# Kernel tuning notes

Measured on AMD Instinct MI355X. Metric: run time of the kernel, lower is better.

Reference implementation:

```python
import jax, jax.numpy as jnp
import numpy as np
from jax import lax

K = 3          # kernel_size
STRIDE = 1
PAD = 1
DIL = 1


def conv2d(x, w, b):
    y = lax.conv_general_dilated(
        x, w, (STRIDE, STRIDE), [(PAD, PAD), (PAD, PAD)],
        rhs_dilation=(DIL, DIL),
        dimension_numbers=('NCHW', 'OIHW', 'NCHW'))
    return y + b[None, :, None, None]


def setup_inputs() -> dict:
    key = jax.random.key(0)
    ks = jax.random.split(key, 6)
    N, Cin, Cout, H, W = 4, 64, 64, 192, 192
    K2 = K * K
    x_input = jax.random.normal(ks[0], (N, Cin, H, W), jnp.float32)
    # offset branch: 2*K2 output channels (dy, dx per kernel tap); small init
    w_off = jax.random.normal(ks[1], (2 * K2, Cin, K, K), jnp.float32) * 0.01
    b_off = jnp.zeros((2 * K2,), jnp.float32)
    # modulation branch (DCNv2): K2 channels, 2*sigmoid
    w_mod = jax.random.normal(ks[2], (K2, Cin, K, K), jnp.float32) * 0.01
    b_mod = jnp.zeros((K2,), jnp.float32)
    # main conv weight + bias
    w = jax.random.normal(ks[3], (Cout, Cin, K, K), jnp.float32) / np.sqrt(Cin * K2)
    b = jax.random.normal(ks[4], (Cout,), jnp.float32) * 0.01
    return {'x_input': x_input, 'w_off': w_off, 'b_off': b_off,
            'w_mod': w_mod, 'b_mod': b_mod, 'w': w, 'b': b}


def _deform_sample(x, py, px):
    # x [N,C,H,W]; py,px [N,K2,Ho,Wo] -> bilinear samples [N,C,K2,Ho,Wo]
    N, C, H, W = x.shape
    xf = x.reshape(N, C, H * W)
    y0 = jnp.floor(py)
    x0 = jnp.floor(px)
    ly = py - y0
    lx = px - x0
    y0i = y0.astype(jnp.int32)
    x0i = x0.astype(jnp.int32)

    def gather(yi, xi, wt):
        valid = (yi >= 0) & (yi < H) & (xi >= 0) & (xi < W)  # zero padding outside
        idx = jnp.clip(yi, 0, H - 1) * W + jnp.clip(xi, 0, W - 1)
        idx_flat = idx.reshape(N, -1)
        vals = jax.vmap(lambda a, i: jnp.take(a, i, axis=1))(xf, idx_flat)  # [N,C,K2*Ho*Wo]
        vals = vals.reshape(N, C, *yi.shape[1:])
        return vals * (wt * valid)[:, None]

    out = gather(y0i, x0i, (1 - ly) * (1 - lx))
    out = out + gather(y0i, x0i + 1, (1 - ly) * lx)
    out = out + gather(y0i + 1, x0i, ly * (1 - lx))
    out = out + gather(y0i + 1, x0i + 1, ly * lx)
    return out


def reference(x_input, w_off, b_off, w_mod, b_mod, w, b):
    N, C, H, W = x_input.shape
    K2 = K * K
    off = conv2d(x_input, w_off, b_off)                       # [N,2*K2,Ho,Wo]
    mod = 2.0 * jax.nn.sigmoid(conv2d(x_input, w_mod, b_mod))  # [N,K2,Ho,Wo]
    Ho, Wo = off.shape[2], off.shape[3]
    off = off.reshape(N, K2, 2, Ho, Wo)
    ky = jnp.repeat(jnp.arange(K) * DIL, K).astype(jnp.float32)  # [K2]
    kx = jnp.tile(jnp.arange(K) * DIL, K).astype(jnp.float32)
    hy = (jnp.arange(Ho) * STRIDE - PAD).astype(jnp.float32)
    wx = (jnp.arange(Wo) * STRIDE - PAD).astype(jnp.float32)
    py = off[:, :, 0] + hy[None, None, :, None] + ky[None, :, None, None]  # [N,K2,Ho,Wo]
    px = off[:, :, 1] + wx[None, None, None, :] + kx[None, :, None, None]
    val = _deform_sample(x_input, py, px) * mod[:, None]       # [N,C,K2,Ho,Wo]
    out = jnp.einsum('nckhw,ock->nohw', val, w.reshape(w.shape[0], C, K2))
    out = out + b[None, :, None, None]
    return jax.nn.relu(out)
```

## Files before the change

kernel.cpp:

```cpp
#include <hip/hip_runtime.h>
#include <hip/hip_bf16.h>
#include <hip/hip_fp16.h>
#include <math.h>


#define NB   4
#define CIN  64
#define COUT 64
#define HH   192
#define WW   192
#define HW   (HH*WW)

typedef __attribute__((ext_vector_type(4))) float f32x4;
typedef __attribute__((ext_vector_type(8))) _Float16 f16x8;
typedef __attribute__((ext_vector_type(4))) unsigned int u32x4;

__device__ __forceinline__ int iclamp(int v, int lo, int hi) {
    return v < lo ? lo : (v > hi ? hi : v);
}
__device__ __forceinline__ unsigned short f16bits(float f) {
    __half h = __float2half(f);
    union { __half h; unsigned short u; } t; t.h = h; return t.u;
}
__device__ __forceinline__ float h2f(unsigned short u) {
    union { unsigned short u; __half h; } t; t.u = u; return __half2float(t.h);
}

__global__ __launch_bounds__(256) void to_nhwc(
        const float* __restrict__ x, unsigned short* __restrict__ xt) {
    int n  = blockIdx.y;
    int px = blockIdx.x * 256 + threadIdx.x;
    const float* xn = x + (size_t)n * CIN * HW + px;
    union { unsigned short us[64]; u32x4 q[8]; } pk;
#pragma unroll
    for (int c = 0; c < 64; c++) pk.us[c] = f16bits(xn[c * HW]);
    u32x4* dst = (u32x4*)(xt + ((size_t)n * HW + px) * 64);
#pragma unroll
    for (int i = 0; i < 8; i++) dst[i] = pk.q[i];
}

__global__ __launch_bounds__(256) void prep_weights(
        const float* __restrict__ w, const float* __restrict__ w_off,
        const float* __restrict__ w_mod, const float* __restrict__ b_off,
        const float* __restrict__ b_mod, unsigned short* __restrict__ wfrag,
        unsigned short* __restrict__ wauxf, float* __restrict__ baux) {
    int idx = blockIdx.x * 256 + threadIdx.x;
    if (idx < 36864) {
        int j    = idx & 7;
        int lane = (idx >> 3) & 63;
        int kc   = (idx >> 9) & 1;
        int g    = (idx >> 10) & 3;
        int k    = idx >> 12;
        int o = g * 16 + (lane & 15);
        int c = kc * 32 + (lane >> 4) * 8 + j;
        wfrag[idx] = f16bits(w[(o * 64 + c) * 9 + k]);
    }
    if (idx < 18432) {
        int j    = idx & 7;
        int lane = (idx >> 3) & 63;
        int kc   = (idx >> 9) & 1;
        int ga   = (idx >> 10) & 1;
        int k    = idx >> 11;
        int o = ga * 16 + (lane & 15);
        int c = kc * 32 + (lane >> 4) * 8 + j;
        float v = 0.f;
        if (o < 18)      v = w_off[(o * 64 + c) * 9 + k];
        else if (o < 27) v = w_mod[((o - 18) * 64 + c) * 9 + k];
        wauxf[idx] = f16bits(v);
    }
    if (idx < 32) {
        float v = 0.f;
        if (idx < 18)      v = b_off[idx];
        else if (idx < 27) v = b_mod[idx - 18];
        baux[idx] = v;
    }
}

__global__ __launch_bounds__(256, 4) void dcn_fused(
        const unsigned short* __restrict__ xt,
        const unsigned short* __restrict__ wfrag,
        const unsigned short* __restrict__ wauxf,
        const float* __restrict__ baux,
        const float* __restrict__ bias,
        float* __restrict__ out) {
    __shared__ __align__(16) unsigned short win[216 * 64];
    __shared__ unsigned short oml[2][32][34];

    int tid = threadIdx.x;
    int l   = tid & 63;
    int wv  = __builtin_amdgcn_readfirstlane(tid >> 6);
    int r2  = wv >> 1;
    int g2  = wv & 1;

    int id = blockIdx.x;
    int sw = (id & 7) * 288 + (id >> 3);
    int n  = sw / 576;
    int r  = sw % 576;
    int ho2    = (r / 6) * 2;
    int wobase = (r % 6) * 32;

    const char* xb = (const char*)xt + (size_t)n * HW * 128;

    if (tid < 216) {
        int rw = tid / 36, cl = tid - rw * 36;
        int gy = iclamp(ho2 - 2 + rw, 0, HH - 1);
        int gx = iclamp(wobase - 2 + cl, 0, WW - 1);
        const u32x4* src = (const u32x4*)(xb + ((size_t)gy * WW + gx) * 128);
        char* dst = (char*)win + tid * 128;
        int xw = (tid & 7) << 4;
#pragma unroll
        for (int c = 0; c < 8; c++)
            *(u32x4*)(dst + ((c * 16) ^ xw)) = src[c];
    }
    __syncthreads();

    {
        f32x4 aacc[2];
        aacc[0] = (f32x4){0.f, 0.f, 0.f, 0.f};
        aacc[1] = (f32x4){0.f, 0.f, 0.f, 0.f};
        const f16x8 zero8 = (f16x8){0, 0, 0, 0, 0, 0, 0, 0};
        int pa   = g2 * 16 + (l & 15);
        int cba  = (l >> 4) * 16;
        int ho_w = ho2 + r2;

#pragma unroll 1
        for (int k = 0; k < 9; k++) {
            int ky = k / 3, kx = k - 3 * (k / 3);
            int ys = ho_w + ky - 1;
            if ((unsigned)ys >= (unsigned)HH) continue;
            int xs = wobase + pa + kx - 1;
            bool ok = (unsigned)xs < (unsigned)WW;
            int sA = (ky + 1 + r2) * 36 + (pa + kx + 1);
            const char* pp = (const char*)win + sA * 128;
            int xw = (sA & 7) << 4;
            const f16x8* wa = ((const f16x8*)wauxf) + (k * 4) * 64 + l;
#pragma unroll
            for (int kc = 0; kc < 2; kc++) {
                f16x8 bv = *(const f16x8*)(pp + ((kc * 64 + cba) ^ xw));
                if (!ok) bv = zero8;
                f16x8 a0 = wa[(kc)     * 64];
                f16x8 a1 = wa[(2 + kc) * 64];
                aacc[0] = __builtin_amdgcn_mfma_f32_16x16x32_f16(a0, bv, aacc[0], 0, 0, 0);
                aacc[1] = __builtin_amdgcn_mfma_f32_16x16x32_f16(a1, bv, aacc[1], 0, 0, 0);
            }
        }
#pragma unroll
        for (int h = 0; h < 2; h++) {
#pragma unroll
            for (int rr = 0; rr < 4; rr++) {
                int o = h * 16 + (l >> 4) * 4 + rr;
                float v = aacc[h][rr] + baux[o];
                if (o >= 18) v = 2.f / (1.f + expf(-v));
                oml[r2][o][pa] = f16bits(v);
            }
        }
    }
    __syncthreads();

    f32x4 acc[4];
#pragma unroll
    for (int nf = 0; nf < 4; nf++) acc[nf] = (f32x4){0.f, 0.f, 0.f, 0.f};

    int p_loc = l & 15;
    int chunk = l >> 4;
    int p     = g2 * 16 + p_loc;
    int ho_w  = ho2 + r2;
    int wox   = wobase + p;
    int cb0   = chunk * 16;

    union Q { u32x4 u; __half2 h2[4]; };

#pragma unroll 1
    for (int k = 0; k < 9; k++) {
        const f16x8* wfk = ((const f16x8*)wfrag) + (k * 8) * 64 + l;
        f16x8 wB[8];
#pragma unroll
        for (int f = 0; f < 8; f++) wB[f] = wfk[f * 64];

        int ky = k / 3, kx = k - 3 * (k / 3);
        float offy = h2f(oml[r2][2 * k][p]);
        float offx = h2f(oml[r2][2 * k + 1][p]);
        float mm   = h2f(oml[r2][18 + k][p]);
        float py  = offy + (float)(ho_w - 1 + ky);
        float pxf = offx + (float)(wox - 1 + kx);
        float y0f = floorf(py), x0f = floorf(pxf);
        float ly = py - y0f, lx = pxf - x0f;
        int y0 = (int)y0f, x0 = (int)x0f;
        int y1 = y0 + 1, x1 = x0 + 1;
        bool y0ok = (unsigned)y0 < (unsigned)HH, y1ok = (unsigned)y1 < (unsigned)HH;
        bool x0ok = (unsigned)x0 < (unsigned)WW, x1ok = (unsigned)x1 < (unsigned)WW;
        float wt0 = (y0ok && x0ok) ? mm * (1.f - ly) * (1.f - lx) : 0.f;
        float wt1 = (y0ok && x1ok) ? mm * (1.f - ly) * lx         : 0.f;
        float wt2 = (y1ok && x0ok) ? mm * ly * (1.f - lx)         : 0.f;
        float wt3 = (y1ok && x1ok) ? mm * ly * lx                 : 0.f;
        int y0c = iclamp(y0, 0, HH - 1), y1c = iclamp(y1, 0, HH - 1);
        int x0c = iclamp(x0, 0, WW - 1), x1c = iclamp(x1, 0, WW - 1);

        int sy0 = y0c - ho2 + 2,    sy1 = y1c - ho2 + 2;
        int sx0 = x0c - wobase + 2, sx1 = x1c - wobase + 2;
        int sy0c = iclamp(sy0, 0, 5),  sy1c = iclamp(sy1, 0, 5);
        int sx0c = iclamp(sx0, 0, 35), sx1c = iclamp(sx1, 0, 35);
        bool fb00 = (wt0 > 0.f) && ((sy0 != sy0c) | (sx0 != sx0c));
        bool fb01 = (wt1 > 0.f) && ((sy0 != sy0c) | (sx1 != sx1c));
        bool fb10 = (wt2 > 0.f) && ((sy1 != sy1c) | (sx0 != sx0c));
        bool fb11 = (wt3 > 0.f) && ((sy1 != sy1c) | (sx1 != sx1c));

        int s00 = sy0c * 36 + sx0c, s01 = sy0c * 36 + sx1c;
        int s10 = sy1c * 36 + sx0c, s11 = sy1c * 36 + sx1c;
        const char* w00 = (const char*)win + s00 * 128;
        const char* w01 = (const char*)win + s01 * 128;
        const char* w10 = (const char*)win + s10 * 128;
        const char* w11 = (const char*)win + s11 * 128;
        int x00 = (s00 & 7) << 4, x01 = (s01 & 7) << 4;
        int x10 = (s10 & 7) << 4, x11 = (s11 & 7) << 4;
        Q q0, q1, q2, q3, q4, q5, q6, q7;
        q0.u = *(const u32x4*)(w00 + ((cb0)      ^ x00));
        q1.u = *(const u32x4*)(w00 + ((cb0 + 64) ^ x00));
        q2.u = *(const u32x4*)(w01 + ((cb0)      ^ x01));
        q3.u = *(const u32x4*)(w01 + ((cb0 + 64) ^ x01));
        q4.u = *(const u32x4*)(w10 + ((cb0)      ^ x10));
        q5.u = *(const u32x4*)(w10 + ((cb0 + 64) ^ x10));
        q6.u = *(const u32x4*)(w11 + ((cb0)      ^ x11));
        q7.u = *(const u32x4*)(w11 + ((cb0 + 64) ^ x11));

        if (__builtin_expect(fb00 | fb01 | fb10 | fb11, 0)) {
            if (fb00) { const char* gp = xb + ((size_t)y0c * WW + x0c) * 128 + cb0;
                        q0.u = *(const u32x4*)gp; q1.u = *(const u32x4*)(gp + 64); }
            if (fb01) { const char* gp = xb + ((size_t)y0c * WW + x1c) * 128 + cb0;
                        q2.u = *(const u32x4*)gp; q3.u = *(const u32x4*)(gp + 64); }
            if (fb10) { const char* gp = xb + ((size_t)y1c * WW + x0c) * 128 + cb0;
                        q4.u = *(const u32x4*)gp; q5.u = *(const u32x4*)(gp + 64); }
            if (fb11) { const char* gp = xb + ((size_t)y1c * WW + x1c) * 128 + cb0;
                        q6.u = *(const u32x4*)gp; q7.u = *(const u32x4*)(gp + 64); }
        }

        __half2 wv0 = __float2half2_rn(wt0);
        __half2 wv1 = __float2half2_rn(wt1);
        __half2 wv2 = __float2half2_rn(wt2);
        __half2 wv3 = __float2half2_rn(wt3);
        union { __half2 h2[4]; f16x8 v; } fA0, fA1;
#pragma unroll
        for (int j = 0; j < 4; j++) {
            __half2 t = __hmul2(q0.h2[j], wv0);
            t = __hfma2(q2.h2[j], wv1, t);
            t = __hfma2(q4.h2[j], wv2, t);
            t = __hfma2(q6.h2[j], wv3, t);
            fA0.h2[j] = t;
            __half2 s = __hmul2(q1.h2[j], wv0);
            s = __hfma2(q3.h2[j], wv1, s);
            s = __hfma2(q5.h2[j], wv2, s);
            s = __hfma2(q7.h2[j], wv3, s);
            fA1.h2[j] = s;
        }

        __builtin_amdgcn_s_setprio(1);
#pragma unroll
        for (int nf = 0; nf < 4; nf++) {
            acc[nf] = __builtin_amdgcn_mfma_f32_16x16x32_f16(fA0.v, wB[nf * 2],     acc[nf], 0, 0, 0);
            acc[nf] = __builtin_amdgcn_mfma_f32_16x16x32_f16(fA1.v, wB[nf * 2 + 1], acc[nf], 0, 0, 0);
        }
        __builtin_amdgcn_s_setprio(0);
    }

#pragma unroll
    for (int nf = 0; nf < 4; nf++) {
        int o = nf * 16 + p_loc;
        float bo = bias[o];
        int wo = wobase + g2 * 16 + chunk * 4;
        float* op = out + (((size_t)n * COUT + o) * HH + ho_w) * WW + wo;
#pragma unroll
        for (int rr = 0; rr < 4; rr++) {
            float v = acc[nf][rr] + bo;
            op[rr] = fmaxf(v, 0.f);
        }
    }
}

extern "C" void kernel_launch(void* const* d_in, const int* in_sizes, int n_in,
                              void* d_out, int out_size, void* d_ws, size_t ws_size,
                              hipStream_t stream) {
    const float* x     = (const float*)d_in[0];
    const float* w_off = (const float*)d_in[1];
    const float* b_off = (const float*)d_in[2];
    const float* w_mod = (const float*)d_in[3];
    const float* b_mod = (const float*)d_in[4];
    const float* w     = (const float*)d_in[5];
    const float* b     = (const float*)d_in[6];
    float* out = (float*)d_out;

    unsigned short* wfrag = (unsigned short*)d_ws;
    unsigned short* wauxf = wfrag + 36864;
    float* baux = (float*)(wauxf + 18432);
    unsigned short* xt = (unsigned short*)(baux + 32);

    to_nhwc<<<dim3(144, NB), dim3(256), 0, stream>>>(x, xt);
    prep_weights<<<dim3(144), dim3(256), 0, stream>>>(w, w_off, w_mod, b_off,
                                                      b_mod, wfrag, wauxf, baux);
    dcn_fused<<<dim3(2304), dim3(256), 0, stream>>>(xt, wfrag, wauxf, baux, b, out);
}
```

Measured before the change: 71.27 us.

## Retile DCN block to 4 rows by 16 columns with coalesced halo load

Each block now covers a 4x16 output tile instead of 2x32, which shrinks the shared-memory halo window from 216 to 160 pixels and cuts redundant halo loads. The window fill is rewritten so all 256 threads load 16-byte chunks across five passes instead of 216 threads each copying a full pixel. Launch bounds rise to 6 blocks per CU for more occupancy, which tightens the register budget and may cause spills.

```diff
diff --git a/kernel.cpp b/kernel.cpp
--- a/kernel.cpp
+++ b/kernel.cpp
@@ -76,41 +76,40 @@
     }
 }
 
-__global__ __launch_bounds__(256, 4) void dcn_fused(
+__global__ __launch_bounds__(256, 6) void dcn_fused(
         const unsigned short* __restrict__ xt,
         const unsigned short* __restrict__ wfrag,
         const unsigned short* __restrict__ wauxf,
         const float* __restrict__ baux,
         const float* __restrict__ bias,
         float* __restrict__ out) {
-    __shared__ __align__(16) unsigned short win[216 * 64];
-    __shared__ unsigned short oml[2][32][34];
+    __shared__ __align__(16) unsigned short win[160 * 64];
+    __shared__ unsigned short oml[4][32][17];
 
     int tid = threadIdx.x;
     int l   = tid & 63;
-    int wv  = __builtin_amdgcn_readfirstlane(tid >> 6);
-    int r2  = wv >> 1;
-    int g2  = wv & 1;
+    int r4  = __builtin_amdgcn_readfirstlane(tid >> 6);
 
     int id = blockIdx.x;
     int sw = (id & 7) * 288 + (id >> 3);
     int n  = sw / 576;
     int r  = sw % 576;
-    int ho2    = (r / 6) * 2;
-    int wobase = (r % 6) * 32;
+    int ho4    = (r / 12) * 4;
+    int wobase = (r % 12) * 16;
 
     const char* xb = (const char*)xt + (size_t)n * HW * 128;
 
-    if (tid < 216) {
-        int rw = tid / 36, cl = tid - rw * 36;
-        int gy = iclamp(ho2 - 2 + rw, 0, HH - 1);
-        int gx = iclamp(wobase - 2 + cl, 0, WW - 1);
-        const u32x4* src = (const u32x4*)(xb + ((size_t)gy * WW + gx) * 128);
-        char* dst = (char*)win + tid * 128;
-        int xw = (tid & 7) << 4;
-#pragma unroll
-        for (int c = 0; c < 8; c++)
-            *(u32x4*)(dst + ((c * 16) ^ xw)) = src[c];
+    {
+        int part = tid & 7;
+#pragma unroll
+        for (int pass = 0; pass < 5; pass++) {
+            int slot = (pass * 256 + tid) >> 3;
+            int rw = slot / 20, cl = slot - rw * 20;
+            int gy = iclamp(ho4 - 2 + rw, 0, HH - 1);
+            int gx = iclamp(wobase - 2 + cl, 0, WW - 1);
+            u32x4 v = *(const u32x4*)(xb + ((size_t)gy * WW + gx) * 128 + part * 16);
+            *(u32x4*)((char*)win + slot * 128 + ((part * 16) ^ ((slot & 7) << 4))) = v;
+        }
     }
     __syncthreads();
 
@@ -119,9 +118,9 @@
         aacc[0] = (f32x4){0.f, 0.f, 0.f, 0.f};
         aacc[1] = (f32x4){0.f, 0.f, 0.f, 0.f};
         const f16x8 zero8 = (f16x8){0, 0, 0, 0, 0, 0, 0, 0};
-        int pa   = g2 * 16 + (l & 15);
+        int pa   = l & 15;
         int cba  = (l >> 4) * 16;
-        int ho_w = ho2 + r2;
+        int ho_w = ho4 + r4;
 
 #pragma unroll 1
         for (int k = 0; k < 9; k++) {
@@ -130,7 +129,7 @@
             if ((unsigned)ys >= (unsigned)HH) continue;
             int xs = wobase + pa + kx - 1;
             bool ok = (unsigned)xs < (unsigned)WW;
-            int sA = (ky + 1 + r2) * 36 + (pa + kx + 1);
+            int sA = (r4 + ky + 1) * 20 + (pa + kx + 1);
             const char* pp = (const char*)win + sA * 128;
             int xw = (sA & 7) << 4;
             const f16x8* wa = ((const f16x8*)wauxf) + (k * 4) * 64 + l;
@@ -151,7 +150,7 @@
                 int o = h * 16 + (l >> 4) * 4 + rr;
                 float v = aacc[h][rr] + baux[o];
                 if (o >= 18) v = 2.f / (1.f + expf(-v));
-                oml[r2][o][pa] = f16bits(v);
+                oml[r4][o][pa] = f16bits(v);
             }
         }
     }
@@ -163,9 +162,8 @@
 
     int p_loc = l & 15;
     int chunk = l >> 4;
-    int p     = g2 * 16 + p_loc;
-    int ho_w  = ho2 + r2;
-    int wox   = wobase + p;
+    int ho_w  = ho4 + r4;
+    int wox   = wobase + p_loc;
     int cb0   = chunk * 16;
 
     union Q { u32x4 u; __half2 h2[4]; };
@@ -178,9 +176,9 @@
         for (int f = 0; f < 8; f++) wB[f] = wfk[f * 64];
 
         int ky = k / 3, kx = k - 3 * (k / 3);
-        float offy = h2f(oml[r2][2 * k][p]);
-        float offx = h2f(oml[r2][2 * k + 1][p]);
-        float mm   = h2f(oml[r2][18 + k][p]);
+        float offy = h2f(oml[r4][2 * k][p_loc]);
+        float offx = h2f(oml[r4][2 * k + 1][p_loc]);
+        float mm   = h2f(oml[r4][18 + k][p_loc]);
         float py  = offy + (float)(ho_w - 1 + ky);
         float pxf = offx + (float)(wox - 1 + kx);
         float y0f = floorf(py), x0f = floorf(pxf);
@@ -196,17 +194,17 @@
         int y0c = iclamp(y0, 0, HH - 1), y1c = iclamp(y1, 0, HH - 1);
         int x0c = iclamp(x0, 0, WW - 1), x1c = iclamp(x1, 0, WW - 1);
 
-        int sy0 = y0c - ho2 + 2,    sy1 = y1c - ho2 + 2;
+        int sy0 = y0c - ho4 + 2,    sy1 = y1c - ho4 + 2;
         int sx0 = x0c - wobase + 2, sx1 = x1c - wobase + 2;
-        int sy0c = iclamp(sy0, 0, 5),  sy1c = iclamp(sy1, 0, 5);
-        int sx0c = iclamp(sx0, 0, 35), sx1c = iclamp(sx1, 0, 35);
+        int sy0c = iclamp(sy0, 0, 7),  sy1c = iclamp(sy1, 0, 7);
+        int sx0c = iclamp(sx0, 0, 19), sx1c = iclamp(sx1, 0, 19);
         bool fb00 = (wt0 > 0.f) && ((sy0 != sy0c) | (sx0 != sx0c));
         bool fb01 = (wt1 > 0.f) && ((sy0 != sy0c) | (sx1 != sx1c));
         bool fb10 = (wt2 > 0.f) && ((sy1 != sy1c) | (sx0 != sx0c));
         bool fb11 = (wt3 > 0.f) && ((sy1 != sy1c) | (sx1 != sx1c));
 
-        int s00 = sy0c * 36 + sx0c, s01 = sy0c * 36 + sx1c;
-        int s10 = sy1c * 36 + sx0c, s11 = sy1c * 36 + sx1c;
+        int s00 = sy0c * 20 + sx0c, s01 = sy0c * 20 + sx1c;
+        int s10 = sy1c * 20 + sx0c, s11 = sy1c * 20 + sx1c;
         const char* w00 = (const char*)win + s00 * 128;
         const char* w01 = (const char*)win + s01 * 128;
         const char* w10 = (const char*)win + s10 * 128;
@@ -266,7 +264,7 @@
     for (int nf = 0; nf < 4; nf++) {
         int o = nf * 16 + p_loc;
         float bo = bias[o];
-        int wo = wobase + g2 * 16 + chunk * 4;
+        int wo = wobase + chunk * 4;
         float* op = out + (((size_t)n * COUT + o) * HH + ho_w) * WW + wo;
 #pragma unroll
         for (int rr = 0; rr < 4; rr++) {
```

After: 134.6 us. +88.9%, slower.

## Software-pipeline bilinear gather one tap ahead of MFMA in deform conv

Applied to the files above, without the earlier changes.

Splits the per-tap loop into a STAGE phase (offset decode, weight computation, LDS gathers) and a CONSUME phase (blend and MFMA). Stages are double-buffered so the gather for tap k+1 is issued before the MFMAs for tap k, with sched_barriers keeping that order. The offset/mask LDS layout is transposed so each pixel's dy,dx pair can be read as one 32-bit load. The extra live registers are covered by lowering launch bounds from 4 to 3 blocks per SIMD, which risks lower occupancy.

```diff
diff --git a/kernel.cpp b/kernel.cpp
--- a/kernel.cpp
+++ b/kernel.cpp
@@ -76,7 +76,99 @@
     }
 }
 
-__global__ __launch_bounds__(256, 4) void dcn_fused(
+union Qreg { u32x4 u; __half2 h2[4]; };
+
+#define STAGE(K, WT, Q) do {                                                  \
+    int k_ = (K);                                                             \
+    int ky_ = k_ / 3, kx_ = k_ - 3 * (k_ / 3);                                \
+    unsigned int oyx_ = *(const unsigned int*)(omp + 2 * k_);                 \
+    float offy_ = h2f((unsigned short)(oyx_ & 0xffffu));                      \
+    float offx_ = h2f((unsigned short)(oyx_ >> 16));                          \
+    float mm_   = h2f(omp[18 + k_]);                                          \
+    float py_  = offy_ + (float)(ho_w - 1 + ky_);                             \
+    float pxf_ = offx_ + (float)(wox - 1 + kx_);                              \
+    float y0f_ = floorf(py_), x0f_ = floorf(pxf_);                            \
+    float ly_ = py_ - y0f_, lx_ = pxf_ - x0f_;                                \
+    int y0_ = (int)y0f_, x0_ = (int)x0f_;                                     \
+    int y1_ = y0_ + 1, x1_ = x0_ + 1;                                         \
+    bool y0ok_ = (unsigned)y0_ < (unsigned)HH, y1ok_ = (unsigned)y1_ < (unsigned)HH; \
+    bool x0ok_ = (unsigned)x0_ < (unsigned)WW, x1ok_ = (unsigned)x1_ < (unsigned)WW; \
+    float wt0_ = (y0ok_ && x0ok_) ? mm_ * (1.f - ly_) * (1.f - lx_) : 0.f;    \
+    float wt1_ = (y0ok_ && x1ok_) ? mm_ * (1.f - ly_) * lx_         : 0.f;    \
+    float wt2_ = (y1ok_ && x0ok_) ? mm_ * ly_ * (1.f - lx_)         : 0.f;    \
+    float wt3_ = (y1ok_ && x1ok_) ? mm_ * ly_ * lx_                 : 0.f;    \
+    WT[0] = __float2half2_rn(wt0_);                                           \
+    WT[1] = __float2half2_rn(wt1_);                                           \
+    WT[2] = __float2half2_rn(wt2_);                                           \
+    WT[3] = __float2half2_rn(wt3_);                                           \
+    int y0c_ = iclamp(y0_, 0, HH - 1), y1c_ = iclamp(y1_, 0, HH - 1);         \
+    int x0c_ = iclamp(x0_, 0, WW - 1), x1c_ = iclamp(x1_, 0, WW - 1);         \
+    int sy0_ = y0c_ - ho2 + 2,    sy1_ = y1c_ - ho2 + 2;                      \
+    int sx0_ = x0c_ - wobase + 2, sx1_ = x1c_ - wobase + 2;                   \
+    int sy0c_ = iclamp(sy0_, 0, 5),  sy1c_ = iclamp(sy1_, 0, 5);              \
+    int sx0c_ = iclamp(sx0_, 0, 35), sx1c_ = iclamp(sx1_, 0, 35);             \
+    bool fb00_ = (wt0_ > 0.f) && ((sy0_ != sy0c_) | (sx0_ != sx0c_));         \
+    bool fb01_ = (wt1_ > 0.f) && ((sy0_ != sy0c_) | (sx1_ != sx1c_));         \
+    bool fb10_ = (wt2_ > 0.f) && ((sy1_ != sy1c_) | (sx0_ != sx0c_));         \
+    bool fb11_ = (wt3_ > 0.f) && ((sy1_ != sy1c_) | (sx1_ != sx1c_));         \
+    int s00_ = sy0c_ * 36 + sx0c_, s01_ = sy0c_ * 36 + sx1c_;                 \
+    int s10_ = sy1c_ * 36 + sx0c_, s11_ = sy1c_ * 36 + sx1c_;                 \
+    const char* w00_ = (const char*)win + s00_ * 128;                         \
+    const char* w01_ = (const char*)win + s01_ * 128;                         \
+    const char* w10_ = (const char*)win + s10_ * 128;                         \
+    const char* w11_ = (const char*)win + s11_ * 128;                         \
+    int x00_ = (s00_ & 7) << 4, x01_ = (s01_ & 7) << 4;                       \
+    int x10_ = (s10_ & 7) << 4, x11_ = (s11_ & 7) << 4;                       \
+    Q[0].u = *(const u32x4*)(w00_ + ((cb0)      ^ x00_));                     \
+    Q[1].u = *(const u32x4*)(w00_ + ((cb0 + 64) ^ x00_));                     \
+    Q[2].u = *(const u32x4*)(w01_ + ((cb0)      ^ x01_));                     \
+    Q[3].u = *(const u32x4*)(w01_ + ((cb0 + 64) ^ x01_));                     \
+    Q[4].u = *(const u32x4*)(w10_ + ((cb0)      ^ x10_));                     \
+    Q[5].u = *(const u32x4*)(w10_ + ((cb0 + 64) ^ x10_));                     \
+    Q[6].u = *(const u32x4*)(w11_ + ((cb0)      ^ x11_));                     \
+    Q[7].u = *(const u32x4*)(w11_ + ((cb0 + 64) ^ x11_));                     \
+    if (__builtin_expect(fb00_ | fb01_ | fb10_ | fb11_, 0)) {                 \
+        if (fb00_) { const char* gp = xb + ((size_t)y0c_ * WW + x0c_) * 128 + cb0; \
+                     Q[0].u = *(const u32x4*)gp; Q[1].u = *(const u32x4*)(gp + 64); } \
+        if (fb01_) { const char* gp = xb + ((size_t)y0c_ * WW + x1c_) * 128 + cb0; \
+                     Q[2].u = *(const u32x4*)gp; Q[3].u = *(const u32x4*)(gp + 64); } \
+        if (fb10_) { const char* gp = xb + ((size_t)y1c_ * WW + x0c_) * 128 + cb0; \
+                     Q[4].u = *(const u32x4*)gp; Q[5].u = *(const u32x4*)(gp + 64); } \
+        if (fb11_) { const char* gp = xb + ((size_t)y1c_ * WW + x1c_) * 128 + cb0; \
+                     Q[6].u = *(const u32x4*)gp; Q[7].u = *(const u32x4*)(gp + 64); } \
+    }                                                                         \
+} while (0)
+
+#define CONSUME(K, WT, Q) do {                                                \
+    int k_ = (K);                                                             \
+    const f16x8* wfk_ = ((const f16x8*)wfrag) + (k_ * 8) * 64 + l;            \
+    f16x8 wB_[8];                                                             \
+    _Pragma("unroll")                                                         \
+    for (int f_ = 0; f_ < 8; ++f_) wB_[f_] = wfk_[f_ * 64];                   \
+    union { __half2 h2[4]; f16x8 v; } fA0_, fA1_;                             \
+    _Pragma("unroll")                                                         \
+    for (int j_ = 0; j_ < 4; ++j_) {                                          \
+        __half2 t_ = __hmul2(Q[0].h2[j_], WT[0]);                             \
+        t_ = __hfma2(Q[2].h2[j_], WT[1], t_);                                 \
+        t_ = __hfma2(Q[4].h2[j_], WT[2], t_);                                 \
+        t_ = __hfma2(Q[6].h2[j_], WT[3], t_);                                 \
+        fA0_.h2[j_] = t_;                                                     \
+        __half2 s_ = __hmul2(Q[1].h2[j_], WT[0]);                             \
+        s_ = __hfma2(Q[3].h2[j_], WT[1], s_);                                 \
+        s_ = __hfma2(Q[5].h2[j_], WT[2], s_);                                 \
+        s_ = __hfma2(Q[7].h2[j_], WT[3], s_);                                 \
+        fA1_.h2[j_] = s_;                                                     \
+    }                                                                         \
+    __builtin_amdgcn_s_setprio(1);                                            \
+    _Pragma("unroll")                                                         \
+    for (int nf_ = 0; nf_ < 4; ++nf_) {                                       \
+        acc[nf_] = __builtin_amdgcn_mfma_f32_16x16x32_f16(fA0_.v, wB_[nf_ * 2],     acc[nf_], 0, 0, 0); \
+        acc[nf_] = __builtin_amdgcn_mfma_f32_16x16x32_f16(fA1_.v, wB_[nf_ * 2 + 1], acc[nf_], 0, 0, 0); \
+    }                                                                         \
+    __builtin_amdgcn_s_setprio(0);                                            \
+} while (0)
+
+__global__ __launch_bounds__(256, 3) void dcn_fused(
         const unsigned short* __restrict__ xt,
         const unsigned short* __restrict__ wfrag,
         const unsigned short* __restrict__ wauxf,
@@ -84,7 +176,7 @@
         const float* __restrict__ bias,
         float* __restrict__ out) {
     __shared__ __align__(16) unsigned short win[216 * 64];
-    __shared__ unsigned short oml[2][32][34];
+    __shared__ __align__(16) unsigned short oml[2][32][32];
 
     int tid = threadIdx.x;
     int l   = tid & 63;
@@ -121,12 +213,12 @@
         const f16x8 zero8 = (f16x8){0, 0, 0, 0, 0, 0, 0, 0};
         int pa   = g2 * 16 + (l & 15);
         int cba  = (l >> 4) * 16;
-        int ho_w = ho2 + r2;
+        int ho_a = ho2 + r2;
 
 #pragma unroll 1
         for (int k = 0; k < 9; k++) {
             int ky = k / 3, kx = k - 3 * (k / 3);
-            int ys = ho_w + ky - 1;
+            int ys = ho_a + ky - 1;
             if ((unsigned)ys >= (unsigned)HH) continue;
             int xs = wobase + pa + kx - 1;
             bool ok = (unsigned)xs < (unsigned)WW;
@@ -151,7 +243,7 @@
                 int o = h * 16 + (l >> 4) * 4 + rr;
                 float v = aacc[h][rr] + baux[o];
                 if (o >= 18) v = 2.f / (1.f + expf(-v));
-                oml[r2][o][pa] = f16bits(v);
+                oml[r2][pa][o] = f16bits(v);
             }
         }
     }
@@ -167,100 +259,24 @@
     int ho_w  = ho2 + r2;
     int wox   = wobase + p;
     int cb0   = chunk * 16;
-
-    union Q { u32x4 u; __half2 h2[4]; };
-
+    const unsigned short* omp = &oml[r2][p][0];
+
+    __half2 wtA[4], wtB[4];
+    Qreg qA[8], qB[8];
+
+    STAGE(0, wtA, qA);
 #pragma unroll 1
-    for (int k = 0; k < 9; k++) {
-        const f16x8* wfk = ((const f16x8*)wfrag) + (k * 8) * 64 + l;
-        f16x8 wB[8];
-#pragma unroll
-        for (int f = 0; f < 8; f++) wB[f] = wfk[f * 64];
-
-        int ky = k / 3, kx = k - 3 * (k / 3);
-        float offy = h2f(oml[r2][2 * k][p]);
-        float offx = h2f(oml[r2][2 * k + 1][p]);
-        float mm   = h2f(oml[r2][18 + k][p]);
-        float py  = offy + (float)(ho_w - 1 + ky);
-        float pxf = offx + (float)(wox - 1 + kx);
-        float y0f = floorf(py), x0f = floorf(pxf);
-        float ly = py - y0f, lx = pxf - x0f;
-        int y0 = (int)y0f, x0 = (int)x0f;
-        int y1 = y0 + 1, x1 = x0 + 1;
-        bool y0ok = (unsigned)y0 < (unsigned)HH, y1ok = (unsigned)y1 < (unsigned)HH;
-        bool x0ok = (unsigned)x0 < (unsigned)WW, x1ok = (unsigned)x1 < (unsigned)WW;
-        float wt0 = (y0ok && x0ok) ? mm * (1.f - ly) * (1.f - lx) : 0.f;
-        float wt1 = (y0ok && x1ok) ? mm * (1.f - ly) * lx         : 0.f;
-        float wt2 = (y1ok && x0ok) ? mm * ly * (1.f - lx)         : 0.f;
-        float wt3 = (y1ok && x1ok) ? mm * ly * lx                 : 0.f;
-        int y0c = iclamp(y0, 0, HH - 1), y1c = iclamp(y1, 0, HH - 1);
-        int x0c = iclamp(x0, 0, WW - 1), x1c = iclamp(x1, 0, WW - 1);
-
-        int sy0 = y0c - ho2 + 2,    sy1 = y1c - ho2 + 2;
-        int sx0 = x0c - wobase + 2, sx1 = x1c - wobase + 2;
-        int sy0c = iclamp(sy0, 0, 5),  sy1c = iclamp(sy1, 0, 5);
-        int sx0c = iclamp(sx0, 0, 35), sx1c = iclamp(sx1, 0, 35);
-        bool fb00 = (wt0 > 0.f) && ((sy0 != sy0c) | (sx0 != sx0c));
-        bool fb01 = (wt1 > 0.f) && ((sy0 != sy0c) | (sx1 != sx1c));
-        bool fb10 = (wt2 > 0.f) && ((sy1 != sy1c) | (sx0 != sx0c));
-        bool fb11 = (wt3 > 0.f) && ((sy1 != sy1c) | (sx1 != sx1c));
-
-        int s00 = sy0c * 36 + sx0c, s01 = sy0c * 36 + sx1c;
-        int s10 = sy1c * 36 + sx0c, s11 = sy1c * 36 + sx1c;
-        const char* w00 = (const char*)win + s00 * 128;
-        const char* w01 = (const char*)win + s01 * 128;
-        const char* w10 = (const char*)win + s10 * 128;
-        const char* w11 = (const char*)win + s11 * 128;
-        int x00 = (s00 & 7) << 4, x01 = (s01 & 7) << 4;
-        int x10 = (s10 & 7) << 4, x11 = (s11 & 7) << 4;
-        Q q0, q1, q2, q3, q4, q5, q6, q7;
-        q0.u = *(const u32x4*)(w00 + ((cb0)      ^ x00));
-        q1.u = *(const u32x4*)(w00 + ((cb0 + 64) ^ x00));
-        q2.u = *(const u32x4*)(w01 + ((cb0)      ^ x01));
-        q3.u = *(const u32x4*)(w01 + ((cb0 + 64) ^ x01));
-        q4.u = *(const u32x4*)(w10 + ((cb0)      ^ x10));
-        q5.u = *(const u32x4*)(w10 + ((cb0 + 64) ^ x10));
-        q6.u = *(const u32x4*)(w11 + ((cb0)      ^ x11));
-        q7.u = *(const u32x4*)(w11 + ((cb0 + 64) ^ x11));
-
-        if (__builtin_expect(fb00 | fb01 | fb10 | fb11, 0)) {
-            if (fb00) { const char* gp = xb + ((size_t)y0c * WW + x0c) * 128 + cb0;
-                        q0.u = *(const u32x4*)gp; q1.u = *(const u32x4*)(gp + 64); }
-            if (fb01) { const char* gp = xb + ((size_t)y0c * WW + x1c) * 128 + cb0;
-                        q2.u = *(const u32x4*)gp; q3.u = *(const u32x4*)(gp + 64); }
-            if (fb10) { const char* gp = xb + ((size_t)y1c * WW + x0c) * 128 + cb0;
-                        q4.u = *(const u32x4*)gp; q5.u = *(const u32x4*)(gp + 64); }
-            if (fb11) { const char* gp = xb + ((size_t)y1c * WW + x1c) * 128 + cb0;
-                        q6.u = *(const u32x4*)gp; q7.u = *(const u32x4*)(gp + 64); }
-        }
-
-        __half2 wv0 = __float2half2_rn(wt0);
-        __half2 wv1 = __float2half2_rn(wt1);
-        __half2 wv2 = __float2half2_rn(wt2);
-        __half2 wv3 = __float2half2_rn(wt3);
-        union { __half2 h2[4]; f16x8 v; } fA0, fA1;
-#pragma unroll
-        for (int j = 0; j < 4; j++) {
-            __half2 t = __hmul2(q0.h2[j], wv0);
-            t = __hfma2(q2.h2[j], wv1, t);
-            t = __hfma2(q4.h2[j], wv2, t);
-            t = __hfma2(q6.h2[j], wv3, t);
-            fA0.h2[j] = t;
-            __half2 s = __hmul2(q1.h2[j], wv0);
-            s = __hfma2(q3.h2[j], wv1, s);
-            s = __hfma2(q5.h2[j], wv2, s);
-            s = __hfma2(q7.h2[j], wv3, s);
-            fA1.h2[j] = s;
-        }
-
-        __builtin_amdgcn_s_setprio(1);
-#pragma unroll
-        for (int nf = 0; nf < 4; nf++) {
-            acc[nf] = __builtin_amdgcn_mfma_f32_16x16x32_f16(fA0.v, wB[nf * 2],     acc[nf], 0, 0, 0);
-            acc[nf] = __builtin_amdgcn_mfma_f32_16x16x32_f16(fA1.v, wB[nf * 2 + 1], acc[nf], 0, 0, 0);
-        }
-        __builtin_amdgcn_s_setprio(0);
-    }
+    for (int kk = 0; kk < 4; ++kk) {
+        int k1 = 2 * kk + 1;
+        int k2 = 2 * kk + 2;
+        STAGE(k1, wtB, qB);
+        __builtin_amdgcn_sched_barrier(0);
+        CONSUME(2 * kk, wtA, qA);
+        STAGE(k2, wtA, qA);
+        __builtin_amdgcn_sched_barrier(0);
+        CONSUME(k1, wtB, qB);
+    }
+    CONSUME(8, wtA, qA);
 
 #pragma unroll
     for (int nf = 0; nf < 4; nf++) {
```

Result: slower. 75.60 us (+6.1%).

## Precompute deformable sampling plan once per pixel-tap in shared memory

Applied to the files above, without the earlier changes.

Before the change, each of the 4 lanes sharing a pixel (one per channel chunk) recomputed the bilinear coordinates, weights and fallback flags for every tap. Now a separate pass computes them once per (pixel, tap) across all 256 threads and stores them in shared memory: packed f16 weights plus signed indices, where a negative index marks a global-memory fallback. The main loop then only loads this plan and gathers. The oml layout is transposed so offsets can be read as packed pairs, and launch bounds drop from 4 to 3 waves per SIMD. The cost is an extra barrier, about 18KB more shared memory and lower occupancy.

```diff
diff --git a/kernel.cpp b/kernel.cpp
--- a/kernel.cpp
+++ b/kernel.cpp
@@ -14,6 +14,7 @@
 typedef __attribute__((ext_vector_type(4))) float f32x4;
 typedef __attribute__((ext_vector_type(8))) _Float16 f16x8;
 typedef __attribute__((ext_vector_type(4))) unsigned int u32x4;
+typedef __attribute__((ext_vector_type(4))) int i32x4;
 
 __device__ __forceinline__ int iclamp(int v, int lo, int hi) {
     return v < lo ? lo : (v > hi ? hi : v);
@@ -24,6 +25,10 @@
 }
 __device__ __forceinline__ float h2f(unsigned short u) {
     union { unsigned short u; __half h; } t; t.u = u; return __half2float(t.h);
+}
+__device__ __forceinline__ unsigned int dup16(float f) {
+    unsigned int b = f16bits(f);
+    return b | (b << 16);
 }
 
 __global__ __launch_bounds__(256) void to_nhwc(
@@ -76,7 +81,7 @@
     }
 }
 
-__global__ __launch_bounds__(256, 4) void dcn_fused(
+__global__ __launch_bounds__(256, 3) void dcn_fused(
         const unsigned short* __restrict__ xt,
         const unsigned short* __restrict__ wfrag,
         const unsigned short* __restrict__ wauxf,
@@ -84,7 +89,9 @@
         const float* __restrict__ bias,
         float* __restrict__ out) {
     __shared__ __align__(16) unsigned short win[216 * 64];
-    __shared__ unsigned short oml[2][32][34];
+    __shared__ __align__(16) unsigned short oml[2][32][32];
+    __shared__ __align__(16) u32x4 planW[576];
+    __shared__ __align__(16) i32x4 planC[576];
 
     int tid = threadIdx.x;
     int l   = tid & 63;
@@ -121,12 +128,12 @@
         const f16x8 zero8 = (f16x8){0, 0, 0, 0, 0, 0, 0, 0};
         int pa   = g2 * 16 + (l & 15);
         int cba  = (l >> 4) * 16;
-        int ho_w = ho2 + r2;
+        int ho_a = ho2 + r2;
 
 #pragma unroll 1
         for (int k = 0; k < 9; k++) {
             int ky = k / 3, kx = k - 3 * (k / 3);
-            int ys = ho_w + ky - 1;
+            int ys = ho_a + ky - 1;
             if ((unsigned)ys >= (unsigned)HH) continue;
             int xs = wobase + pa + kx - 1;
             bool ok = (unsigned)xs < (unsigned)WW;
@@ -147,42 +154,34 @@
 #pragma unroll
         for (int h = 0; h < 2; h++) {
 #pragma unroll
-            for (int rr = 0; rr < 4; rr++) {
-                int o = h * 16 + (l >> 4) * 4 + rr;
-                float v = aacc[h][rr] + baux[o];
-                if (o >= 18) v = 2.f / (1.f + expf(-v));
-                oml[r2][o][pa] = f16bits(v);
+            for (int rr = 0; rr < 2; rr++) {
+                int o = h * 16 + (l >> 4) * 4 + rr * 2;
+                float v0 = aacc[h][rr * 2]     + baux[o];
+                float v1 = aacc[h][rr * 2 + 1] + baux[o + 1];
+                if (o     >= 18) v0 = 2.f / (1.f + expf(-v0));
+                if (o + 1 >= 18) v1 = 2.f / (1.f + expf(-v1));
+                unsigned int pk = (unsigned int)f16bits(v0)
+                                | ((unsigned int)f16bits(v1) << 16);
+                *(unsigned int*)&oml[r2][pa][o] = pk;
             }
         }
     }
     __syncthreads();
 
-    f32x4 acc[4];
-#pragma unroll
-    for (int nf = 0; nf < 4; nf++) acc[nf] = (f32x4){0.f, 0.f, 0.f, 0.f};
-
-    int p_loc = l & 15;
-    int chunk = l >> 4;
-    int p     = g2 * 16 + p_loc;
-    int ho_w  = ho2 + r2;
-    int wox   = wobase + p;
-    int cb0   = chunk * 16;
-
-    union Q { u32x4 u; __half2 h2[4]; };
-
-#pragma unroll 1
-    for (int k = 0; k < 9; k++) {
-        const f16x8* wfk = ((const f16x8*)wfrag) + (k * 8) * 64 + l;
-        f16x8 wB[8];
-#pragma unroll
-        for (int f = 0; f < 8; f++) wB[f] = wfk[f * 64];
+    for (int i = tid; i < 576; i += 256) {
+        int rp = i / 9;
+        int k  = i - rp * 9;
+        int r2p = rp >> 5, px = rp & 31;
+        int ho_p  = ho2 + r2p;
+        int wox_p = wobase + px;
 
         int ky = k / 3, kx = k - 3 * (k / 3);
-        float offy = h2f(oml[r2][2 * k][p]);
-        float offx = h2f(oml[r2][2 * k + 1][p]);
-        float mm   = h2f(oml[r2][18 + k][p]);
-        float py  = offy + (float)(ho_w - 1 + ky);
-        float pxf = offx + (float)(wox - 1 + kx);
+        unsigned int oyx = *(const unsigned int*)&oml[r2p][px][2 * k];
+        float offy = h2f((unsigned short)(oyx & 0xffffu));
+        float offx = h2f((unsigned short)(oyx >> 16));
+        float mm   = h2f(oml[r2p][px][18 + k]);
+        float py  = offy + (float)(ho_p - 1 + ky);
+        float pxf = offx + (float)(wox_p - 1 + kx);
         float y0f = floorf(py), x0f = floorf(pxf);
         float ly = py - y0f, lx = pxf - x0f;
         int y0 = (int)y0f, x0 = (int)x0f;
@@ -195,61 +194,92 @@
         float wt3 = (y1ok && x1ok) ? mm * ly * lx                 : 0.f;
         int y0c = iclamp(y0, 0, HH - 1), y1c = iclamp(y1, 0, HH - 1);
         int x0c = iclamp(x0, 0, WW - 1), x1c = iclamp(x1, 0, WW - 1);
-
         int sy0 = y0c - ho2 + 2,    sy1 = y1c - ho2 + 2;
         int sx0 = x0c - wobase + 2, sx1 = x1c - wobase + 2;
         int sy0c = iclamp(sy0, 0, 5),  sy1c = iclamp(sy1, 0, 5);
         int sx0c = iclamp(sx0, 0, 35), sx1c = iclamp(sx1, 0, 35);
-        bool fb00 = (wt0 > 0.f) && ((sy0 != sy0c) | (sx0 != sx0c));
-        bool fb01 = (wt1 > 0.f) && ((sy0 != sy0c) | (sx1 != sx1c));
-        bool fb10 = (wt2 > 0.f) && ((sy1 != sy1c) | (sx0 != sx0c));
-        bool fb11 = (wt3 > 0.f) && ((sy1 != sy1c) | (sx1 != sx1c));
-
-        int s00 = sy0c * 36 + sx0c, s01 = sy0c * 36 + sx1c;
-        int s10 = sy1c * 36 + sx0c, s11 = sy1c * 36 + sx1c;
-        const char* w00 = (const char*)win + s00 * 128;
-        const char* w01 = (const char*)win + s01 * 128;
-        const char* w10 = (const char*)win + s10 * 128;
-        const char* w11 = (const char*)win + s11 * 128;
-        int x00 = (s00 & 7) << 4, x01 = (s01 & 7) << 4;
-        int x10 = (s10 & 7) << 4, x11 = (s11 & 7) << 4;
+        bool fb0 = (wt0 > 0.f) && ((sy0 != sy0c) | (sx0 != sx0c));
+        bool fb1 = (wt1 > 0.f) && ((sy0 != sy0c) | (sx1 != sx1c));
+        bool fb2 = (wt2 > 0.f) && ((sy1 != sy1c) | (sx0 != sx0c));
+        bool fb3 = (wt3 > 0.f) && ((sy1 != sy1c) | (sx1 != sx1c));
+        int c0 = fb0 ? -(y0c * WW + x0c) - 1 : sy0c * 36 + sx0c;
+        int c1 = fb1 ? -(y0c * WW + x1c) - 1 : sy0c * 36 + sx1c;
+        int c2 = fb2 ? -(y1c * WW + x0c) - 1 : sy1c * 36 + sx0c;
+        int c3 = fb3 ? -(y1c * WW + x1c) - 1 : sy1c * 36 + sx1c;
+
+        planW[i] = (u32x4){dup16(wt0), dup16(wt1), dup16(wt2), dup16(wt3)};
+        planC[i] = (i32x4){c0, c1, c2, c3};
+    }
+    __syncthreads();
+
+    f32x4 acc[4];
+#pragma unroll
+    for (int nf = 0; nf < 4; nf++) acc[nf] = (f32x4){0.f, 0.f, 0.f, 0.f};
+
+    int p_loc = l & 15;
+    int chunk = l >> 4;
+    int p     = g2 * 16 + p_loc;
+    int ho_w  = ho2 + r2;
+    int cb0   = chunk * 16;
+    int cb1   = cb0 + 64;
+    const char* planWp = (const char*)planW + (r2 * 32 + p) * 9 * 16;
+    const char* planCp = (const char*)planC + (r2 * 32 + p) * 9 * 16;
+
+    union Q { u32x4 u; __half2 h2[4]; };
+
+#pragma unroll 1
+    for (int k = 0; k < 9; k++) {
+        const f16x8* wfk = ((const f16x8*)wfrag) + (k * 8) * 64 + l;
+        f16x8 wB[8];
+#pragma unroll
+        for (int f = 0; f < 8; f++) wB[f] = wfk[f * 64];
+
+        union { u32x4 u; __half2 h2[4]; } pw;
+        pw.u = *(const u32x4*)(planWp + k * 16);
+        i32x4 pc = *(const i32x4*)(planCp + k * 16);
+        int c0 = pc.x, c1 = pc.y, c2 = pc.z, c3 = pc.w;
+
+        int d0 = c0 < 0 ? 0 : c0, d1 = c1 < 0 ? 0 : c1;
+        int d2 = c2 < 0 ? 0 : c2, d3 = c3 < 0 ? 0 : c3;
+        const char* b0 = (const char*)win + d0 * 128;
+        const char* b1 = (const char*)win + d1 * 128;
+        const char* b2 = (const char*)win + d2 * 128;
+        const char* b3 = (const char*)win + d3 * 128;
+        int x0 = (d0 & 7) << 4, x1 = (d1 & 7) << 4;
+        int x2 = (d2 & 7) << 4, x3 = (d3 & 7) << 4;
         Q q0, q1, q2, q3, q4, q5, q6, q7;
-        q0.u = *(const u32x4*)(w00 + ((cb0)      ^ x00));
-        q1.u = *(const u32x4*)(w00 + ((cb0 + 64) ^ x00));
-        q2.u = *(const u32x4*)(w01 + ((cb0)      ^ x01));
-        q3.u = *(const u32x4*)(w01 + ((cb0 + 64) ^ x01));
-        q4.u = *(const u32x4*)(w10 + ((cb0)      ^ x10));
-        q5.u = *(const u32x4*)(w10 + ((cb0 + 64) ^ x10));
-        q6.u = *(const u32x4*)(w11 + ((cb0)      ^ x11));
-        q7.u = *(const u32x4*)(w11 + ((cb0 + 64) ^ x11));
-
-        if (__builtin_expect(fb00 | fb01 | fb10 | fb11, 0)) {
-            if (fb00) { const char* gp = xb + ((size_t)y0c * WW + x0c) * 128 + cb0;
-                        q0.u = *(const u32x4*)gp; q1.u = *(const u32x4*)(gp + 64); }
-            if (fb01) { const char* gp = xb + ((size_t)y0c * WW + x1c) * 128 + cb0;
-                        q2.u = *(const u32x4*)gp; q3.u = *(const u32x4*)(gp + 64); }
-            if (fb10) { const char* gp = xb + ((size_t)y1c * WW + x0c) * 128 + cb0;
-                        q4.u = *(const u32x4*)gp; q5.u = *(const u32x4*)(gp + 64); }
-            if (fb11) { const char* gp = xb + ((size_t)y1c * WW + x1c) * 128 + cb0;
-                        q6.u = *(const u32x4*)gp; q7.u = *(const u32x4*)(gp + 64); }
-        }
-
-        __half2 wv0 = __float2half2_rn(wt0);
-        __half2 wv1 = __float2half2_rn(wt1);
-        __half2 wv2 = __float2half2_rn(wt2);
-        __half2 wv3 = __float2half2_rn(wt3);
+        q0.u = *(const u32x4*)(b0 + (cb0 ^ x0));
+        q1.u = *(const u32x4*)(b0 + (cb1 ^ x0));
+        q2.u = *(const u32x4*)(b1 + (cb0 ^ x1));
+        q3.u = *(const u32x4*)(b1 + (cb1 ^ x1));
+        q4.u = *(const u32x4*)(b2 + (cb0 ^ x2));
+        q5.u = *(const u32x4*)(b2 + (cb1 ^ x2));
+        q6.u = *(const u32x4*)(b3 + (cb0 ^ x3));
+        q7.u = *(const u32x4*)(b3 + (cb1 ^ x3));
+
+        if (__builtin_expect((c0 | c1 | c2 | c3) < 0, 0)) {
+            if (c0 < 0) { const char* gp = xb + (size_t)(-c0 - 1) * 128 + cb0;
+                          q0.u = *(const u32x4*)gp; q1.u = *(const u32x4*)(gp + 64); }
+            if (c1 < 0) { const char* gp = xb + (size_t)(-c1 - 1) * 128 + cb0;
+                          q2.u = *(const u32x4*)gp; q3.u = *(const u32x4*)(gp + 64); }
+            if (c2 < 0) { const char* gp = xb + (size_t)(-c2 - 1) * 128 + cb0;
+                          q4.u = *(const u32x4*)gp; q5.u = *(const u32x4*)(gp + 64); }
+            if (c3 < 0) { const char* gp = xb + (size_t)(-c3 - 1) * 128 + cb0;
+                          q6.u = *(const u32x4*)gp; q7.u = *(const u32x4*)(gp + 64); }
+        }
+
         union { __half2 h2[4]; f16x8 v; } fA0, fA1;
 #pragma unroll
         for (int j = 0; j < 4; j++) {
-            __half2 t = __hmul2(q0.h2[j], wv0);
-            t = __hfma2(q2.h2[j], wv1, t);
-            t = __hfma2(q4.h2[j], wv2, t);
-            t = __hfma2(q6.h2[j], wv3, t);
+            __half2 t = __hmul2(q0.h2[j], pw.h2[0]);
+            t = __hfma2(q2.h2[j], pw.h2[1], t);
+            t = __hfma2(q4.h2[j], pw.h2[2], t);
+            t = __hfma2(q6.h2[j], pw.h2[3], t);
             fA0.h2[j] = t;
-            __half2 s = __hmul2(q1.h2[j], wv0);
-            s = __hfma2(q3.h2[j], wv1, s);
-            s = __hfma2(q5.h2[j], wv2, s);
-            s = __hfma2(q7.h2[j], wv3, s);
+            __half2 s = __hmul2(q1.h2[j], pw.h2[0]);
+            s = __hfma2(q3.h2[j], pw.h2[1], s);
+            s = __hfma2(q5.h2[j], pw.h2[2], s);
+            s = __hfma2(q7.h2[j], pw.h2[3], s);
             fA1.h2[j] = s;
         }
 
```

Result: no change. 72.43 us (+1.6%).
